# Kernel optimization log

Measured on AMD Instinct MI355X. Metric: run time of the kernel, lower is better.

Reference implementation:

```python
import jax, jax.numpy as jnp
import numpy as np
import math

N, E, LAT, MUL, HD = 20000, 160000, 128, 16, 32
H = LAT // HD          # 4 heads
D = 9                  # 0e+1o+2e spherical harmonics dim
SLICES = ((0, 1), (1, 4), (4, 9))
TPD = MUL * len(SLICES)


def _mlp(x, W1, b1, W2, b2):
    return jnp.dot(jax.nn.silu(jnp.dot(x, W1) + b1), W2) + b2


def _eq_linear(x, W):
    # block-diagonal per-l channel mixing: x [E, mul, D], W [n_l, mul, mul]
    return jnp.concatenate([jnp.einsum('ji,eim->ejm', W[l], x[:, :, s:t])
                            for l, (s, t) in enumerate(SLICES)], axis=-1)


def _residual(x, x_new, uc):
    co = jax.lax.rsqrt(uc * uc + 1.0)
    return co * x + (uc * co) * x_new


def _vec_rej(feat, dirs):
    d = dirs[:, None, :]
    return feat - (feat * d).sum(-1, keepdims=True) * d


def _so3_ln(x, eps=1e-8):
    # equivariant RMS layernorm per irrep block
    out = []
    for s, t in SLICES:
        blk = x[:, :, s:t]
        rms = jnp.sqrt((blk * blk).sum(-1).mean(-1) + eps)  # [N]
        out.append(blk / rms[:, None, None])
    return jnp.concatenate(out, axis=-1)


def _ln(x, g, b, eps=1e-5):
    mu = x.mean(-1, keepdims=True)
    var = ((x - mu) ** 2).mean(-1, keepdims=True)
    return (x - mu) * jax.lax.rsqrt(var + eps) * g + b


def _forward(h, X, t_ij, spharms, update_coeff, Wtq, Wtk, Wrs_W, Wrs_b, Wq_W, Wq_b, Wk_W, Wk_b, Wre_W, ln_g, ln_b, Wvu,
             gs_W1, gs_b1, gs_W2, gs_b2, gv_W1, gv_b1, gv_W2, gv_b2, gw_W1, gw_b1, gw_W2, gw_b2,
             gt_W1, gt_b1, gt_W2, gt_b2, gsp_W1, gsp_b1, gsp_W2, gsp_b2, md_W1, md_b1, md_W2, md_b2,
             mt_W1, mt_b1, mt_W2, mt_b2, gm_W1, gm_b1, gm_W2, gm_b2,
             edge_center, edge_neighbor, num_nodes):
    uc = update_coeff
    Xn = X[edge_neighbor]                                     # [E, mul, D]
    Xq = _vec_rej(_eq_linear(X[edge_center], Wtq), spharms)
    Xk = _vec_rej(_eq_linear(Xn, Wtk), -spharms)
    # CG scalar contraction (l x l -> 0e, uuu): normalized per-l dot product
    w = jnp.concatenate([(Xq[:, :, s:t] * Xk[:, :, s:t]).sum(-1) / math.sqrt(t - s)
                         for s, t in SLICES], axis=-1)        # [E, 3*mul]
    dt = _mlp(w, gw_W1, gw_b1, gw_W2, gw_b2) * _mlp(t_ij, gt_W1, gt_b1, gt_W2, gt_b2)
    t_ij = _residual(t_ij, dt, uc)
    h_i = h[edge_center]
    h_j = h[edge_neighbor]
    spatial = (t_ij @ Wrs_W + Wrs_b) * _mlp(h_j, gs_W1, gs_b1, gs_W2, gs_b2)
    En = t_ij.shape[0]
    q = (h_i @ Wq_W + Wq_b).reshape(En, H, HD)
    k = (h_j @ Wk_W + Wk_b).reshape(En, H, HD)
    v = _mlp(h_j, gv_W1, gv_b1, gv_W2, gv_b2)
    ta = jax.nn.silu(t_ij @ Wre_W).reshape(En, H, HD)
    alpha = (q * k * ta).sum(-1) / math.sqrt(HD)              # [E, H]
    amax = jax.ops.segment_max(alpha, edge_center, num_segments=num_nodes)
    ex = jnp.exp(alpha - amax[edge_center])
    den = jax.ops.segment_sum(ex, edge_center, num_segments=num_nodes)
    attn = ex / den[edge_center]                              # scatter_softmax
    sea = (attn[:, :, None] * v.reshape(En, H, HD)).reshape(En, LAT)
    combined = sea + spatial
    gates = _mlp(combined, gsp_W1, gsp_b1, gsp_W2, gsp_b2)
    o_s, o_d, o_t = gates[:, :LAT], gates[:, LAT:2 * LAT], gates[:, 2 * LAT:]
    dh = _ln(jax.ops.segment_sum(o_s, edge_center, num_segments=num_nodes), ln_g, ln_b)
    h = _residual(h, dh, uc)
    gd = _mlp(o_d, md_W1, md_b1, md_W2, md_b2)
    gtt = _mlp(o_t, mt_W1, mt_b1, mt_W2, mt_b2)
    dXij = gd[:, :, None] * spharms[:, None, :] + gtt[:, :, None] * Xn
    dX = _so3_ln(jax.ops.segment_sum(dXij, edge_center, num_segments=num_nodes))
    X = _residual(X, dX, uc)
    # EQFF
    Xp = jnp.einsum('nmi,mj->nji', X, Wvu)
    nrm = jnp.sqrt((Xp * Xp).sum(-1) + 1e-12)
    g = _mlp(jnp.concatenate([h, nrm], axis=-1), gm_W1, gm_b1, gm_W2, gm_b2)
    h = h + g[:, :LAT]
    X = X + g[:, LAT:, None] * Xp
    return h, X, t_ij


def setup_inputs() -> dict:
    key = jax.random.key(0)
    ks = jax.random.split(key, 24)

    def mk_mlp(k, din, dout):
        k1, k2 = jax.random.split(k)
        return (jax.random.normal(k1, (din, LAT)) / math.sqrt(din), jnp.zeros((LAT,)),
                jax.random.normal(k2, (LAT, dout)) / math.sqrt(LAT), jnp.zeros((dout,)))

    inp = {
        'h': jax.random.normal(ks[0], (N, LAT)),
        'X': jax.random.normal(ks[1], (N, MUL, D)),
        't_ij': jax.random.normal(ks[2], (E, LAT)),
        'spharms': jax.random.normal(ks[3], (E, D)),
        'update_coeff': jnp.ones((1,), dtype=jnp.float32),
        'Wtq': jax.random.normal(ks[4], (len(SLICES), MUL, MUL)) / math.sqrt(MUL),
        'Wtk': jax.random.normal(ks[5], (len(SLICES), MUL, MUL)) / math.sqrt(MUL),
        'Wrs_W': jax.random.normal(ks[6], (LAT, LAT)) / math.sqrt(LAT),
        'Wrs_b': jnp.zeros((LAT,)),
        'Wq_W': jax.random.normal(ks[7], (LAT, LAT)) / math.sqrt(LAT),
        'Wq_b': jnp.zeros((LAT,)),
        'Wk_W': jax.random.normal(ks[8], (LAT, LAT)) / math.sqrt(LAT),
        'Wk_b': jnp.zeros((LAT,)),
        'Wre_W': jax.random.normal(ks[9], (LAT, LAT)) / math.sqrt(LAT),
        'ln_g': jnp.ones((LAT,)),
        'ln_b': jnp.zeros((LAT,)),
        'Wvu': jax.random.normal(ks[10], (MUL, MUL)) / math.sqrt(MUL),
    }
    for name, din, dout, k in [('gs', LAT, LAT, ks[11]), ('gv', LAT, LAT, ks[12]), ('gw', TPD, LAT, ks[13]),
                               ('gt', LAT, LAT, ks[14]), ('gsp', LAT, 3 * LAT, ks[15]), ('md', LAT, MUL, ks[16]),
                               ('mt', LAT, MUL, ks[17]), ('gm', LAT + MUL, LAT + MUL, ks[18])]:
        W1, b1, W2, b2 = mk_mlp(k, din, dout)
        inp[name + '_W1'], inp[name + '_b1'], inp[name + '_W2'], inp[name + '_b2'] = W1, b1, W2, b2
    inp['edge_center'] = jax.random.randint(ks[19], (E,), 0, N)
    inp['edge_neighbor'] = jax.random.randint(ks[20], (E,), 0, N)
    inp['num_nodes'] = N
    return inp


def reference(h, X, t_ij, spharms, update_coeff, Wtq, Wtk, Wrs_W, Wrs_b, Wq_W, Wq_b, Wk_W, Wk_b, Wre_W, ln_g, ln_b, Wvu,
              gs_W1, gs_b1, gs_W2, gs_b2, gv_W1, gv_b1, gv_W2, gv_b2, gw_W1, gw_b1, gw_W2, gw_b2,
              gt_W1, gt_b1, gt_W2, gt_b2, gsp_W1, gsp_b1, gsp_W2, gsp_b2, md_W1, md_b1, md_W2, md_b2,
              mt_W1, mt_b1, mt_W2, mt_b2, gm_W1, gm_b1, gm_W2, gm_b2,
              edge_center, edge_neighbor, num_nodes):
    return _forward(h, X, t_ij, spharms, update_coeff, Wtq, Wtk, Wrs_W, Wrs_b, Wq_W, Wq_b, Wk_W, Wk_b, Wre_W, ln_g, ln_b, Wvu,
                    gs_W1, gs_b1, gs_W2, gs_b2, gv_W1, gv_b1, gv_W2, gv_b2, gw_W1, gw_b1, gw_W2, gw_b2,
                    gt_W1, gt_b1, gt_W2, gt_b2, gsp_W1, gsp_b1, gsp_W2, gsp_b2, md_W1, md_b1, md_W2, md_b2,
                    mt_W1, mt_b1, mt_W2, mt_b2, gm_W1, gm_b1, gm_W2, gm_b2,
                    edge_center, edge_neighbor, num_nodes)
```

## Files before the change

kernel.cpp:

```cpp
#include <hip/hip_runtime.h>
#include <math.h>

#define N_NODES 20000
#define E_EDGES 160000
#define LAT 128
#define MUL 16
#define DD 9
#define TPD 48

#define WS_Q      ((size_t)0)
#define WS_K      (WS_Q + (size_t)N_NODES*LAT)
#define WS_V      (WS_K + (size_t)N_NODES*LAT)
#define WS_S      (WS_V + (size_t)N_NODES*LAT)
#define WS_W48    (WS_S + (size_t)N_NODES*LAT)
#define WS_SPATB  (WS_W48 + (size_t)E_EDGES*TPD)
#define WS_ALPHA  (WS_SPATB + (size_t)E_EDGES*LAT/2)
#define WS_ZERO   (WS_ALPHA + (size_t)E_EDGES*4)
#define WS_AMAX   WS_ZERO
#define WS_DEN    (WS_AMAX + (size_t)N_NODES*4)
#define WS_HSUM   (WS_DEN + (size_t)N_NODES*4)
#define WS_NDX    (WS_HSUM + (size_t)N_NODES*LAT)
#define WS_END    (WS_NDX + (size_t)N_NODES*MUL*DD)
#define ZERO_CNT  (WS_END - WS_ZERO)
#define WS_WB     WS_END

#define WOFF_WQ   0
#define WOFF_WK   16384
#define WOFF_GV1  32768
#define WOFF_GV2  49152
#define WOFF_GS1  65536
#define WOFF_GS2  81920
#define WOFF_GW1  98304
#define WOFF_GW2  106496
#define WOFF_GT1  122880
#define WOFF_GT2  139264
#define WOFF_WRS  155648
#define WOFF_WRE  172032
#define WOFF_GSP1 188416
#define WOFF_GSP2 204800
#define WOFF_MD1  253952
#define WOFF_MD2  270336
#define WOFF_MT1  272384
#define WOFF_MT2  288768
#define WB_TOTAL  290816

#define DEVI __device__ __forceinline__

typedef short short8 __attribute__((ext_vector_type(8)));
typedef float f32x4 __attribute__((ext_vector_type(4)));

DEVI float silu_f(float x){ return x / (1.f + expf(-x)); }
DEVI unsigned int fmap(float x){ unsigned int b=__float_as_uint(x); return (b&0x80000000u)? ~b : (b|0x80000000u); }
DEVI float funmap(unsigned int u){ return (u&0x80000000u)? __uint_as_float(u&0x7fffffffu) : __uint_as_float(~u); }
DEVI unsigned short f2b(float f){ unsigned int u=__float_as_uint(f); return (unsigned short)((u + 0x7fffu + ((u>>16)&1u))>>16); }
DEVI float b2f(unsigned short u){ return __uint_as_float(((unsigned int)u)<<16); }

DEVI f32x4 mfma16(short8 a, short8 b, f32x4 c){
  return __builtin_amdgcn_mfma_f32_16x16x32_bf16(a,b,c,0,0,0);
}

template<int KB>
DEVI void mm_tile2(const unsigned short* act, int strideUS, const unsigned short* Wp,
                   int ntile, int m, int quad, f32x4* acc){
  const unsigned short* wp = Wp + (size_t)ntile*KB*512 + (size_t)quad*128 + m*8;
  const unsigned short* a0 = act + m*strideUS + quad*8;
  const unsigned short* a1 = a0 + 16*strideUS;
  #pragma unroll
  for (int kb=0;kb<KB;++kb){
    short8 bfr = *(const short8*)(wp + (size_t)kb*512);
    short8 af0 = *(const short8*)(a0 + kb*32);
    short8 af1 = *(const short8*)(a1 + kb*32);
    acc[0]=mfma16(af0,bfr,acc[0]);
    acc[1]=mfma16(af1,bfr,acc[1]);
  }
}

template<int KB>
DEVI void mm_tile1(const unsigned short* act, int strideUS, const unsigned short* Wp,
                   int mtbase, int m, int quad, f32x4& acc){
  const unsigned short* wp = Wp + (size_t)quad*128 + m*8;
  const unsigned short* a0 = act + (mtbase*16+m)*strideUS + quad*8;
  #pragma unroll
  for (int kb=0;kb<KB;++kb){
    short8 bfr = *(const short8*)(wp + (size_t)kb*512);
    short8 af  = *(const short8*)(a0 + kb*32);
    acc=mfma16(af,bfr,acc);
  }
}

template<int R, int KD, int LDSTRIDE>
DEVI void mm_acc(const float* src, const float* __restrict__ W, int wstride, int t, float* acc){
  #pragma unroll 2
  for (int k=0;k<KD;k+=4){
    float4 xv[R];
    #pragma unroll
    for (int r=0;r<R;++r) xv[r] = *(const float4*)(src + r*LDSTRIDE + k);
    #pragma unroll
    for (int kk=0;kk<4;++kk){
      float wk = W[(size_t)(k+kk)*wstride + t];
      #pragma unroll
      for (int r=0;r<R;++r) acc[r] += ((const float*)&xv[r])[kk]*wk;
    }
  }
}

__global__ void k0_zero(float* __restrict__ z){
  size_t i = (size_t)blockIdx.x*256 + threadIdx.x;
  if (i < ZERO_CNT) z[i] = 0.f;
}

__global__ __launch_bounds__(256) void k_pack(
  const float* __restrict__ Wq,const float* __restrict__ Wk,
  const float* __restrict__ gv1,const float* __restrict__ gv2,
  const float* __restrict__ gs1,const float* __restrict__ gs2,
  const float* __restrict__ gw1,const float* __restrict__ gw2,
  const float* __restrict__ gt1,const float* __restrict__ gt2,
  const float* __restrict__ Wrs,const float* __restrict__ Wre,
  const float* __restrict__ gsp1,const float* __restrict__ gsp2,
  const float* __restrict__ md1,const float* __restrict__ md2,
  const float* __restrict__ mt1,const float* __restrict__ mt2,
  unsigned short* __restrict__ dst)
{
  int i = blockIdx.x*256 + threadIdx.x;
  if (i >= WB_TOTAL) return;
  const int off[19] = {0,16384,32768,49152,65536,81920,98304,106496,122880,139264,
                       155648,172032,188416,204800,253952,270336,272384,288768,290816};
  int mi=0;
  while (i >= off[mi+1]) ++mi;
  int li = i - off[mi];
  int N = (mi==13)?384:((mi==15||mi==17)?16:128);
  int Ksrc = (mi==6)?48:128;
  int KB = (mi==6)?2:4;
  int j = li&7; int t = li>>3;
  int n_in = t&15; t>>=4;
  int quad = t&3; t>>=2;
  int k_block = t % KB; int n_tile = t / KB;
  int k = k_block*32 + quad*8 + j;
  int n = n_tile*16 + n_in;
  const float* src;
  switch(mi){
    case 0: src=Wq; break;  case 1: src=Wk; break;
    case 2: src=gv1; break; case 3: src=gv2; break;
    case 4: src=gs1; break; case 5: src=gs2; break;
    case 6: src=gw1; break; case 7: src=gw2; break;
    case 8: src=gt1; break; case 9: src=gt2; break;
    case 10: src=Wrs; break; case 11: src=Wre; break;
    case 12: src=gsp1; break; case 13: src=gsp2; break;
    case 14: src=md1; break; case 15: src=md2; break;
    default: src=(mi==16)?mt1:mt2; break;
  }
  float v = (k < Ksrc) ? src[(size_t)k*N + n] : 0.f;
  dst[i] = f2b(v);
}

__global__ __launch_bounds__(256) void k1_node(const float* __restrict__ h,
  const unsigned short* __restrict__ WB,
  const float* __restrict__ Wq_b,const float* __restrict__ Wk_b,
  const float* __restrict__ gv_b1,const float* __restrict__ gv_b2,
  const float* __restrict__ gs_b1,const float* __restrict__ gs_b2,
  float* __restrict__ ws)
{
  __shared__ __align__(16) unsigned short B0[32*136], B1[32*136];
  const int tid=threadIdx.x, lane=tid&63, w=tid>>6, m=lane&15, quad=lane>>4;
  const int n0=blockIdx.x*32;
  for (int idx=tid; idx<4096; idx+=256){ int r=idx>>7,c=idx&127;
    B0[r*136+c]=f2b(h[(size_t)(n0+r)*128+c]); }
  __syncthreads();
  f32x4 z4 = {0.f,0.f,0.f,0.f};
  { f32x4 acc[2][2]={{z4,z4},{z4,z4}};
    #pragma unroll
    for(int i=0;i<2;++i) mm_tile2<4>(B0,136,WB+WOFF_WQ, w*2+i, m, quad, acc[i]);
    #pragma unroll
    for(int i=0;i<2;++i){ int col=(w*2+i)*16+m; float bv=Wq_b[col];
      #pragma unroll
      for(int mt=0;mt<2;++mt)
        #pragma unroll
        for(int r=0;r<4;++r){ int row=mt*16+quad*4+r;
          ws[WS_Q+(size_t)(n0+row)*128+col]=acc[i][mt][r]+bv; } } }
  { f32x4 acc[2][2]={{z4,z4},{z4,z4}};
    #pragma unroll
    for(int i=0;i<2;++i) mm_tile2<4>(B0,136,WB+WOFF_WK, w*2+i, m, quad, acc[i]);
    #pragma unroll
    for(int i=0;i<2;++i){ int col=(w*2+i)*16+m; float bv=Wk_b[col];
      #pragma unroll
      for(int mt=0;mt<2;++mt)
        #pragma unroll
        for(int r=0;r<4;++r){ int row=mt*16+quad*4+r;
          ws[WS_K+(size_t)(n0+row)*128+col]=acc[i][mt][r]+bv; } } }
  { f32x4 acc[2][2]={{z4,z4},{z4,z4}};
    #pragma unroll
    for(int i=0;i<2;++i) mm_tile2<4>(B0,136,WB+WOFF_GV1, w*2+i, m, quad, acc[i]);
    #pragma unroll
    for(int i=0;i<2;++i){ int col=(w*2+i)*16+m; float bv=gv_b1[col];
      #pragma unroll
      for(int mt=0;mt<2;++mt)
        #pragma unroll
        for(int r=0;r<4;++r) B1[(mt*16+quad*4+r)*136+col]=f2b(silu_f(acc[i][mt][r]+bv)); } }
  __syncthreads();
  { f32x4 acc[2][2]={{z4,z4},{z4,z4}};
    #pragma unroll
    for(int i=0;i<2;++i) mm_tile2<4>(B1,136,WB+WOFF_GV2, w*2+i, m, quad, acc[i]);
    #pragma unroll
    for(int i=0;i<2;++i){ int col=(w*2+i)*16+m; float bv=gv_b2[col];
      #pragma unroll
      for(int mt=0;mt<2;++mt)
        #pragma unroll
        for(int r=0;r<4;++r){ int row=mt*16+quad*4+r;
          ws[WS_V+(size_t)(n0+row)*128+col]=acc[i][mt][r]+bv; } } }
  __syncthreads();
  { f32x4 acc[2][2]={{z4,z4},{z4,z4}};
    #pragma unroll
    for(int i=0;i<2;++i) mm_tile2<4>(B0,136,WB+WOFF_GS1, w*2+i, m, quad, acc[i]);
    #pragma unroll
    for(int i=0;i<2;++i){ int col=(w*2+i)*16+m; float bv=gs_b1[col];
      #pragma unroll
      for(int mt=0;mt<2;++mt)
        #pragma unroll
        for(int r=0;r<4;++r) B1[(mt*16+quad*4+r)*136+col]=f2b(silu_f(acc[i][mt][r]+bv)); } }
  __syncthreads();
  { f32x4 acc[2][2]={{z4,z4},{z4,z4}};
    #pragma unroll
    for(int i=0;i<2;++i) mm_tile2<4>(B1,136,WB+WOFF_GS2, w*2+i, m, quad, acc[i]);
    #pragma unroll
    for(int i=0;i<2;++i){ int col=(w*2+i)*16+m; float bv=gs_b2[col];
      #pragma unroll
      for(int mt=0;mt<2;++mt)
        #pragma unroll
        for(int r=0;r<4;++r){ int row=mt*16+quad*4+r;
          ws[WS_S+(size_t)(n0+row)*128+col]=acc[i][mt][r]+bv; } } }
}

__global__ __launch_bounds__(256) void k2_edge_w(
  const float* __restrict__ Xin, const float* __restrict__ sph,
  const float* __restrict__ Wtq, const float* __restrict__ Wtk,
  const int* __restrict__ ec, const int* __restrict__ en, float* __restrict__ ws)
{
  __shared__ float xc[16][144], xn[16][144], sphL[16][9];
  __shared__ float wq[768], wkk[768];
  __shared__ int ceI[16], nbI[16];
  const int tid=threadIdx.x, e0=blockIdx.x*16;
  if (tid<16){ ceI[tid]=ec[e0+tid]; nbI[tid]=en[e0+tid]; }
  for (int idx=tid; idx<768; idx+=256){ wq[idx]=Wtq[idx]; wkk[idx]=Wtk[idx]; }
  __syncthreads();
  for (int idx=tid; idx<2304; idx+=256){ int r=idx/144,c=idx%144;
    xc[r][c]=Xin[(size_t)ceI[r]*144+c]; xn[r][c]=Xin[(size_t)nbI[r]*144+c]; }
  if (tid<144){ int r=tid/9,c=tid%9; sphL[r][c]=sph[(size_t)(e0+r)*9+c]; }
  __syncthreads();
  const int el=tid>>4, j=tid&15;
  float xq[9], xk[9];
  const int ss[3]={0,1,4}, se[3]={1,4,9};
  #pragma unroll
  for (int l=0;l<3;++l){
    for (int mm2=ss[l]; mm2<se[l]; ++mm2){
      float aq=0.f, ak=0.f;
      #pragma unroll
      for (int i=0;i<16;++i){
        float wql = wq[l*256 + j*16 + i], wkl = wkk[l*256 + j*16 + i];
        aq += wql*xc[el][i*9+mm2];
        ak += wkl*xn[el][i*9+mm2];
      }
      xq[mm2]=aq; xk[mm2]=ak;
    }
  }
  float dq=0.f, dk=0.f;
  #pragma unroll
  for (int d=0; d<9; ++d){ dq += xq[d]*sphL[el][d]; dk += xk[d]*sphL[el][d]; }
  #pragma unroll
  for (int d=0; d<9; ++d){ xq[d] -= dq*sphL[el][d]; xk[d] -= dk*sphL[el][d]; }
  const float isc[3] = {1.f, 0.5773502691896258f, 0.4472135954999579f};
  #pragma unroll
  for (int l=0;l<3;++l){
    float s=0.f;
    for (int mm2=ss[l]; mm2<se[l]; ++mm2) s += xq[mm2]*xk[mm2];
    ws[WS_W48 + (size_t)(e0+el)*TPD + l*16 + j] = s*isc[l];
  }
}

__global__ __launch_bounds__(256) void k3_edge_t(
  const float* __restrict__ t_in, const int* __restrict__ ec, const int* __restrict__ en,
  const unsigned short* __restrict__ WB,
  const float* __restrict__ gw_b1,const float* __restrict__ gw_b2,
  const float* __restrict__ gt_b1,const float* __restrict__ gt_b2,
  const float* __restrict__ Wrs_b,
  const float* __restrict__ ucp, float* __restrict__ ws, float* __restrict__ outT)
{
  __shared__ __align__(16) unsigned short tin_b[32*136], hid_b[32*136], tnw_b[32*136], wb_b[32*72];
  __shared__ float qk[32*132];
  __shared__ int ceI[32], nbI[32];
  const int tid=threadIdx.x, lane=tid&63, w=tid>>6, m=lane&15, quad=lane>>4;
  const int e0=blockIdx.x*32;
  if (tid<32){ ceI[tid]=ec[e0+tid]; nbI[tid]=en[e0+tid]; }
  __syncthreads();
  const float* Qp=ws+WS_Q; const float* Kp=ws+WS_K;
  for (int idx=tid; idx<4096; idx+=256){
    int r=idx>>7, c=idx&127;
    tin_b[r*136+c] = f2b(t_in[(size_t)(e0+r)*128+c]);
    qk[r*132+c] = Qp[(size_t)ceI[r]*128+c]*Kp[(size_t)nbI[r]*128+c];
  }
  for (int idx=tid; idx<2048; idx+=256){
    int r=idx>>6, c=idx&63;
    wb_b[r*72+c] = (c<48)? f2b(ws[WS_W48+(size_t)(e0+r)*TPD+c]) : (unsigned short)0;
  }
  __syncthreads();
  const float uc=ucp[0], co=rsqrtf(uc*uc+1.f), ucco=uc*co;
  f32x4 z4 = {0.f,0.f,0.f,0.f};
  { f32x4 acc[2][2]={{z4,z4},{z4,z4}};
    #pragma unroll
    for(int i=0;i<2;++i) mm_tile2<2>(wb_b,72,WB+WOFF_GW1, w*2+i, m, quad, acc[i]);
    #pragma unroll
    for(int i=0;i<2;++i){ int col=(w*2+i)*16+m; float bv=gw_b1[col];
      #pragma unroll
      for(int mt=0;mt<2;++mt)
        #pragma unroll
        for(int r=0;r<4;++r) hid_b[(mt*16+quad*4+r)*136+col]=f2b(silu_f(acc[i][mt][r]+bv)); } }
  __syncthreads();
  f32x4 accw[2][2]={{z4,z4},{z4,z4}};
  #pragma unroll
  for(int i=0;i<2;++i) mm_tile2<4>(hid_b,136,WB+WOFF_GW2, w*2+i, m, quad, accw[i]);
  __syncthreads();
  { f32x4 acc[2][2]={{z4,z4},{z4,z4}};
    #pragma unroll
    for(int i=0;i<2;++i) mm_tile2<4>(tin_b,136,WB+WOFF_GT1, w*2+i, m, quad, acc[i]);
    #pragma unroll
    for(int i=0;i<2;++i){ int col=(w*2+i)*16+m; float bv=gt_b1[col];
      #pragma unroll
      for(int mt=0;mt<2;++mt)
        #pragma unroll
        for(int r=0;r<4;++r) hid_b[(mt*16+quad*4+r)*136+col]=f2b(silu_f(acc[i][mt][r]+bv)); } }
  __syncthreads();
  { f32x4 acct[2][2]={{z4,z4},{z4,z4}};
    #pragma unroll
    for(int i=0;i<2;++i) mm_tile2<4>(hid_b,136,WB+WOFF_GT2, w*2+i, m, quad, acct[i]);
    #pragma unroll
    for(int i=0;i<2;++i){ int col=(w*2+i)*16+m; float bw=gw_b2[col], bt=gt_b2[col];
      #pragma unroll
      for(int mt=0;mt<2;++mt)
        #pragma unroll
        for(int r=0;r<4;++r){ int row=mt*16+quad*4+r;
          float dt=(accw[i][mt][r]+bw)*(acct[i][mt][r]+bt);
          float tn=co*b2f(tin_b[row*136+col]) + ucco*dt;
          tnw_b[row*136+col]=f2b(tn);
          outT[(size_t)(e0+row)*128+col]=tn; } } }
  __syncthreads();
  unsigned short* spatB = (unsigned short*)(ws+WS_SPATB);
  { f32x4 acc[2][2]={{z4,z4},{z4,z4}};
    #pragma unroll
    for(int i=0;i<2;++i) mm_tile2<4>(tnw_b,136,WB+WOFF_WRS, w*2+i, m, quad, acc[i]);
    #pragma unroll
    for(int i=0;i<2;++i){ int col=(w*2+i)*16+m; float bv=Wrs_b[col];
      #pragma unroll
      for(int mt=0;mt<2;++mt)
        #pragma unroll
        for(int r=0;r<4;++r){ int row=mt*16+quad*4+r;
          float sv=ws[WS_S+(size_t)nbI[row]*128+col];
          spatB[(size_t)(e0+row)*128+col]=f2b((acc[i][mt][r]+bv)*sv); } } }
  { f32x4 acc[2][2]={{z4,z4},{z4,z4}};
    #pragma unroll
    for(int i=0;i<2;++i) mm_tile2<4>(tnw_b,136,WB+WOFF_WRE, w*2+i, m, quad, acc[i]);
    unsigned int* amaxu=(unsigned int*)(ws+WS_AMAX);
    #pragma unroll
    for(int mt=0;mt<2;++mt)
      #pragma unroll
      for(int r=0;r<4;++r){ int row=mt*16+quad*4+r;
        float p=0.f;
        #pragma unroll
        for(int i=0;i<2;++i){ int col=(w*2+i)*16+m;
          p += qk[row*132+col]*silu_f(acc[i][mt][r]); }
        p += __shfl_xor(p,1); p += __shfl_xor(p,2); p += __shfl_xor(p,4); p += __shfl_xor(p,8);
        if (m==0){
          float aval = p * 0.17677669529663687f;
          int e=e0+row;
          ws[WS_ALPHA+(size_t)e*4+w]=aval;
          atomicMax(&amaxu[(size_t)ceI[row]*4+w], fmap(aval));
        } } }
}

__global__ __launch_bounds__(256) void k4_softmax(const int* __restrict__ ec, float* __restrict__ ws){
  int i = blockIdx.x*256 + threadIdx.x;
  if (i >= E_EDGES*4) return;
  int e = i>>2, hh = i&3;
  int c = ec[e];
  float a = ws[WS_ALPHA + i];
  const unsigned int* amaxu = (const unsigned int*)(ws + WS_AMAX);
  float am = funmap(amaxu[(size_t)c*4+hh]);
  float exv = expf(a - am);
  ws[WS_ALPHA + i] = exv;
  atomicAdd(&ws[WS_DEN + (size_t)c*4 + hh], exv);
}

__global__ __launch_bounds__(256) void k5_edge_gate(
  const float* __restrict__ Xin, const float* __restrict__ sph,
  const int* __restrict__ ec, const int* __restrict__ en,
  const unsigned short* __restrict__ WB,
  const float* __restrict__ gsp_b1,const float* __restrict__ gsp_b2,
  const float* __restrict__ md_b1,const float* __restrict__ md_b2,
  const float* __restrict__ mt_b1,const float* __restrict__ mt_b2,
  float* __restrict__ ws)
{
  __shared__ __align__(16) unsigned short B0[32*136], B1[32*136], B2[32*136], B3[32*136];
  __shared__ float gdL[32*16], gtL[32*16], attnL[32*4];
  __shared__ int ceI[32], nbI[32];
  const int tid=threadIdx.x, lane=tid&63, w=tid>>6, m=lane&15, quad=lane>>4;
  const int e0=blockIdx.x*32;
  if (tid<32){ ceI[tid]=ec[e0+tid]; nbI[tid]=en[e0+tid]; }
  __syncthreads();
  if (tid<128){ int r=tid>>2, hh=tid&3;
    attnL[tid] = ws[WS_ALPHA+(size_t)(e0+r)*4+hh] / ws[WS_DEN+(size_t)ceI[r]*4+hh]; }
  __syncthreads();
  const float* Vp=ws+WS_V;
  const unsigned short* spatB=(const unsigned short*)(ws+WS_SPATB);
  for (int idx=tid; idx<4096; idx+=256){ int r=idx>>7,c=idx&127;
    float v = attnL[r*4+(c>>5)]*Vp[(size_t)nbI[r]*128+c] + b2f(spatB[(size_t)(e0+r)*128+c]);
    B0[r*136+c]=f2b(v); }
  __syncthreads();
  f32x4 z4 = {0.f,0.f,0.f,0.f};
  { f32x4 acc[2][2]={{z4,z4},{z4,z4}};
    #pragma unroll
    for(int i=0;i<2;++i) mm_tile2<4>(B0,136,WB+WOFF_GSP1, w*2+i, m, quad, acc[i]);
    #pragma unroll
    for(int i=0;i<2;++i){ int col=(w*2+i)*16+m; float bv=gsp_b1[col];
      #pragma unroll
      for(int mt=0;mt<2;++mt)
        #pragma unroll
        for(int r=0;r<4;++r) B1[(mt*16+quad*4+r)*136+col]=f2b(silu_f(acc[i][mt][r]+bv)); } }
  __syncthreads();
  { f32x4 acc[3][2][2];
    #pragma unroll
    for(int g2=0;g2<3;++g2)
      #pragma unroll
      for(int i=0;i<2;++i){ acc[g2][i][0]=z4; acc[g2][i][1]=z4; }
    #pragma unroll
    for(int g2=0;g2<3;++g2)
      #pragma unroll
      for(int i=0;i<2;++i)
        mm_tile2<4>(B1,136,WB+WOFF_GSP2, g2*8+w*2+i, m, quad, acc[g2][i]);
    float* hsum=ws+WS_HSUM;
    #pragma unroll
    for(int i=0;i<2;++i){ int col=(w*2+i)*16+m;
      float bS=gsp_b2[col], bD=gsp_b2[128+col], bT=gsp_b2[256+col];
      #pragma unroll
      for(int mt=0;mt<2;++mt)
        #pragma unroll
        for(int r=0;r<4;++r){ int row=mt*16+quad*4+r;
          atomicAdd(&hsum[(size_t)ceI[row]*128+col], acc[0][i][mt][r]+bS);
          B2[row*136+col]=f2b(acc[1][i][mt][r]+bD);
          B3[row*136+col]=f2b(acc[2][i][mt][r]+bT); } } }
  __syncthreads();
  { f32x4 acc[2][2]={{z4,z4},{z4,z4}};
    #pragma unroll
    for(int i=0;i<2;++i) mm_tile2<4>(B2,136,WB+WOFF_MD1, w*2+i, m, quad, acc[i]);
    #pragma unroll
    for(int i=0;i<2;++i){ int col=(w*2+i)*16+m; float bv=md_b1[col];
      #pragma unroll
      for(int mt=0;mt<2;++mt)
        #pragma unroll
        for(int r=0;r<4;++r) B0[(mt*16+quad*4+r)*136+col]=f2b(silu_f(acc[i][mt][r]+bv)); } }
  __syncthreads();
  { f32x4 acc[2][2]={{z4,z4},{z4,z4}};
    #pragma unroll
    for(int i=0;i<2;++i) mm_tile2<4>(B3,136,WB+WOFF_MT1, w*2+i, m, quad, acc[i]);
    #pragma unroll
    for(int i=0;i<2;++i){ int col=(w*2+i)*16+m; float bv=mt_b1[col];
      #pragma unroll
      for(int mt=0;mt<2;++mt)
        #pragma unroll
        for(int r=0;r<4;++r) B2[(mt*16+quad*4+r)*136+col]=f2b(silu_f(acc[i][mt][r]+bv)); } }
  __syncthreads();
  { if (w<2){
      f32x4 a=z4; mm_tile1<4>(B0,136,WB+WOFF_MD2, w, m, quad, a);
      #pragma unroll
      for(int r=0;r<4;++r) gdL[(w*16+quad*4+r)*16+m]=a[r]+md_b2[m];
    } else {
      f32x4 a=z4; mm_tile1<4>(B2,136,WB+WOFF_MT2, w-2, m, quad, a);
      #pragma unroll
      for(int r=0;r<4;++r) gtL[((w-2)*16+quad*4+r)*16+m]=a[r]+mt_b2[m];
    } }
  __syncthreads();
  float* ndx=ws+WS_NDX;
  for (int idx=tid; idx<4608; idx+=256){
    int r=idx/144, c=idx-r*144; int mm2=c/9, d=c-mm2*9;
    float val = gdL[r*16+mm2]*sph[(size_t)(e0+r)*9+d] + gtL[r*16+mm2]*Xin[(size_t)nbI[r]*144+c];
    atomicAdd(&ndx[(size_t)ceI[r]*144+c], val);
  }
}

__global__ __launch_bounds__(128) void k6_node(
  const float* __restrict__ h, const float* __restrict__ Xin,
  const float* __restrict__ ln_g,const float* __restrict__ ln_b,
  const float* __restrict__ Wvu,
  const float* __restrict__ gm_W1,const float* __restrict__ gm_b1,
  const float* __restrict__ gm_W2,const float* __restrict__ gm_b2,
  const float* __restrict__ ucp, const float* __restrict__ ws,
  float* __restrict__ outH, float* __restrict__ outX)
{
  __shared__ float cat[4][144], dxb[4][144], xnw[4][144], xp[4][144], hid[4][LAT];
  __shared__ float red[4][2][2], rinv[4][3], gX[4][16], wvu[256];
  const int t=threadIdx.x, n0=blockIdx.x*4;
  const float* hsum=ws+WS_HSUM; const float* ndx=ws+WS_NDX;
  const float uc=ucp[0], co=rsqrtf(uc*uc+1.f), ucco=uc*co;
  for (int idx=t; idx<256; idx+=128) wvu[idx]=Wvu[idx];
  for (int idx=t; idx<576; idx+=128){ int r=idx/144,c=idx%144; dxb[r][c]=ndx[(size_t)(n0+r)*144+c]; }
  float xv_[4];
  #pragma unroll
  for (int r=0;r<4;++r){
    float x=hsum[(size_t)(n0+r)*LAT+t]; xv_[r]=x;
    float s=x, ss=x*x;
    for (int off=32; off; off>>=1){ s+=__shfl_down(s,off,64); ss+=__shfl_down(ss,off,64); }
    if ((t&63)==0){ red[r][t>>6][0]=s; red[r][t>>6][1]=ss; }
  }
  __syncthreads();
  #pragma unroll
  for (int r=0;r<4;++r){
    float s=red[r][0][0]+red[r][1][0], ss=red[r][0][1]+red[r][1][1];
    float mu=s*(1.f/128.f), var=ss*(1.f/128.f)-mu*mu;
    float dh=(xv_[r]-mu)*rsqrtf(var+1e-5f)*ln_g[t]+ln_b[t];
    cat[r][t]=co*h[(size_t)(n0+r)*LAT+t]+ucco*dh;
  }
  if (t<12){
    int r=t/3, l=t-r*3;
    int s0 = (l==0)?0:((l==1)?1:4);
    int s1 = (l==0)?1:((l==1)?4:9);
    float sum=0.f;
    for (int mm2=0;mm2<16;++mm2)
      for (int d=s0;d<s1;++d){ float v=dxb[r][mm2*9+d]; sum+=v*v; }
    rinv[r][l]=rsqrtf(sum*(1.f/16.f)+1e-8f);
  }
  __syncthreads();
  for (int idx=t; idx<144; idx+=128){
    int d=idx%9; int l=(d==0)?0:((d<4)?1:2);
    #pragma unroll
    for (int r=0;r<4;++r)
      xnw[r][idx]=co*Xin[(size_t)(n0+r)*144+idx]+ucco*dxb[r][idx]*rinv[r][l];
  }
  __syncthreads();
  for (int idx=t; idx<144; idx+=128){
    int j=idx/9, i=idx-j*9;
    #pragma unroll
    for (int r=0;r<4;++r){
      float a=0.f;
      #pragma unroll
      for (int mm2=0;mm2<16;++mm2) a+=xnw[r][mm2*9+i]*wvu[mm2*16+j];
      xp[r][idx]=a;
    }
  }
  __syncthreads();
  if (t<64){ int r=t>>4, j=t&15; float s=1e-12f;
    #pragma unroll
    for (int i=0;i<9;++i){ float v=xp[r][j*9+i]; s+=v*v; }
    cat[r][128+j]=sqrtf(s); }
  __syncthreads();
  { float acc[4]; float b=gm_b1[t];
    #pragma unroll
    for(int r=0;r<4;++r)acc[r]=b;
    mm_acc<4,144,144>(&cat[0][0],gm_W1,LAT,t,acc);
    #pragma unroll
    for(int r=0;r<4;++r) hid[r][t]=silu_f(acc[r]); }
  __syncthreads();
  { float acc[4]; float b=gm_b2[t];
    #pragma unroll
    for(int r=0;r<4;++r)acc[r]=b;
    mm_acc<4,LAT,LAT>(&hid[0][0],gm_W2,144,t,acc);
    #pragma unroll
    for(int r=0;r<4;++r) outH[(size_t)(n0+r)*LAT+t]=cat[r][t]+acc[r]; }
  if (t<16){ float acc[4]; float b=gm_b2[128+t];
    #pragma unroll
    for(int r=0;r<4;++r)acc[r]=b;
    for (int k=0;k<LAT;++k){ float wk=gm_W2[(size_t)k*144+128+t];
      #pragma unroll
      for(int r=0;r<4;++r) acc[r]+=hid[r][k]*wk; }
    #pragma unroll
    for(int r=0;r<4;++r) gX[r][t]=acc[r]; }
  __syncthreads();
  for (int idx=t; idx<144; idx+=128){
    int j=idx/9;
    #pragma unroll
    for (int r=0;r<4;++r)
      outX[(size_t)(n0+r)*144+idx]=xnw[r][idx]+gX[r][j]*xp[r][idx];
  }
}

extern "C" void kernel_launch(void* const* d_in, const int* in_sizes, int n_in,
                              void* d_out, int out_size, void* d_ws, size_t ws_size,
                              hipStream_t stream)
{
  const float* h      = (const float*)d_in[0];
  const float* X      = (const float*)d_in[1];
  const float* t_ij   = (const float*)d_in[2];
  const float* sph    = (const float*)d_in[3];
  const float* ucp    = (const float*)d_in[4];
  const float* Wtq    = (const float*)d_in[5];
  const float* Wtk    = (const float*)d_in[6];
  const float* Wrs_W  = (const float*)d_in[7];
  const float* Wrs_b  = (const float*)d_in[8];
  const float* Wq_W   = (const float*)d_in[9];
  const float* Wq_b   = (const float*)d_in[10];
  const float* Wk_W   = (const float*)d_in[11];
  const float* Wk_b   = (const float*)d_in[12];
  const float* Wre_W  = (const float*)d_in[13];
  const float* ln_g   = (const float*)d_in[14];
  const float* ln_b   = (const float*)d_in[15];
  const float* Wvu    = (const float*)d_in[16];
  const float* gs_W1=(const float*)d_in[17], *gs_b1=(const float*)d_in[18],
             *gs_W2=(const float*)d_in[19], *gs_b2=(const float*)d_in[20];
  const float* gv_W1=(const float*)d_in[21], *gv_b1=(const float*)d_in[22],
             *gv_W2=(const float*)d_in[23], *gv_b2=(const float*)d_in[24];
  const float* gw_W1=(const float*)d_in[25], *gw_b1=(const float*)d_in[26],
             *gw_W2=(const float*)d_in[27], *gw_b2=(const float*)d_in[28];
  const float* gt_W1=(const float*)d_in[29], *gt_b1=(const float*)d_in[30],
             *gt_W2=(const float*)d_in[31], *gt_b2=(const float*)d_in[32];
  const float* gsp_W1=(const float*)d_in[33], *gsp_b1=(const float*)d_in[34],
             *gsp_W2=(const float*)d_in[35], *gsp_b2=(const float*)d_in[36];
  const float* md_W1=(const float*)d_in[37], *md_b1=(const float*)d_in[38],
             *md_W2=(const float*)d_in[39], *md_b2=(const float*)d_in[40];
  const float* mt_W1=(const float*)d_in[41], *mt_b1=(const float*)d_in[42],
             *mt_W2=(const float*)d_in[43], *mt_b2=(const float*)d_in[44];
  const float* gm_W1=(const float*)d_in[45], *gm_b1=(const float*)d_in[46],
             *gm_W2=(const float*)d_in[47], *gm_b2=(const float*)d_in[48];
  const int* ec = (const int*)d_in[49];
  const int* en = (const int*)d_in[50];
  (void)in_sizes; (void)n_in; (void)out_size; (void)ws_size;

  float* ws   = (float*)d_ws;
  unsigned short* WB = (unsigned short*)(ws + WS_WB);
  float* outH = (float*)d_out;
  float* outX = outH + (size_t)N_NODES*LAT;
  float* outT = outX + (size_t)N_NODES*MUL*DD;

  k0_zero<<<dim3((unsigned)((ZERO_CNT+255)/256)), dim3(256), 0, stream>>>(ws + WS_ZERO);
  k_pack<<<dim3((WB_TOTAL+255)/256), dim3(256), 0, stream>>>(
      Wq_W,Wk_W, gv_W1,gv_W2, gs_W1,gs_W2, gw_W1,gw_W2, gt_W1,gt_W2,
      Wrs_W,Wre_W, gsp_W1,gsp_W2, md_W1,md_W2, mt_W1,mt_W2, WB);
  k1_node<<<dim3(N_NODES/32), dim3(256), 0, stream>>>(h, WB, Wq_b, Wk_b,
      gv_b1,gv_b2, gs_b1,gs_b2, ws);
  k2_edge_w<<<dim3(E_EDGES/16), dim3(256), 0, stream>>>(X, sph, Wtq, Wtk, ec, en, ws);
  k3_edge_t<<<dim3(E_EDGES/32), dim3(256), 0, stream>>>(t_ij, ec, en, WB,
      gw_b1,gw_b2, gt_b1,gt_b2, Wrs_b, ucp, ws, outT);
  k4_softmax<<<dim3((E_EDGES*4)/256), dim3(256), 0, stream>>>(ec, ws);
  k5_edge_gate<<<dim3(E_EDGES/32), dim3(256), 0, stream>>>(X, sph, ec, en, WB,
      gsp_b1,gsp_b2, md_b1,md_b2, mt_b1,mt_b2, ws);
  k6_node<<<dim3(N_NODES/4), dim3(128), 0, stream>>>(h, X, ln_g, ln_b, Wvu,
      gm_W1,gm_b1,gm_W2,gm_b2, ucp, ws, outH, outX);
}
```

Before: 813.4 us.

## Accumulate node scatter sums with packed bf16 atomics and use fast exp

The hsum and ndx scatter reductions change from fp32 atomicAdd to packed bf16x2 global atomics. Each atomic now carries two adjacent columns, which halves the atomic count and the bytes of contended traffic. The node kernel reads the accumulators back as bf16. silu and softmax also switch to __expf. Summing many edges into bf16 accumulators loses a lot of precision and may break the tolerance check.

```diff
diff --git a/kernel.cpp b/kernel.cpp
--- a/kernel.cpp
+++ b/kernel.cpp
@@ -49,11 +49,15 @@
 typedef short short8 __attribute__((ext_vector_type(8)));
 typedef float f32x4 __attribute__((ext_vector_type(4)));
 
-DEVI float silu_f(float x){ return x / (1.f + expf(-x)); }
+DEVI float silu_f(float x){ return x / (1.f + __expf(-x)); }
 DEVI unsigned int fmap(float x){ unsigned int b=__float_as_uint(x); return (b&0x80000000u)? ~b : (b|0x80000000u); }
 DEVI float funmap(unsigned int u){ return (u&0x80000000u)? __uint_as_float(u&0x7fffffffu) : __uint_as_float(~u); }
 DEVI unsigned short f2b(float f){ unsigned int u=__float_as_uint(f); return (unsigned short)((u + 0x7fffu + ((u>>16)&1u))>>16); }
 DEVI float b2f(unsigned short u){ return __uint_as_float(((unsigned int)u)<<16); }
+
+DEVI void atom_pk(unsigned short* p, unsigned int pk){
+  asm volatile("global_atomic_pk_add_bf16 %0, %1, off" :: "v"(p), "v"(pk) : "memory");
+}
 
 DEVI f32x4 mfma16(short8 a, short8 b, f32x4 c){
   return __builtin_amdgcn_mfma_f32_16x16x32_bf16(a,b,c,0,0,0);
@@ -383,7 +387,7 @@
   float a = ws[WS_ALPHA + i];
   const unsigned int* amaxu = (const unsigned int*)(ws + WS_AMAX);
   float am = funmap(amaxu[(size_t)c*4+hh]);
-  float exv = expf(a - am);
+  float exv = __expf(a - am);
   ws[WS_ALPHA + i] = exv;
   atomicAdd(&ws[WS_DEN + (size_t)c*4 + hh], exv);
 }
@@ -434,7 +438,7 @@
       #pragma unroll
       for(int i=0;i<2;++i)
         mm_tile2<4>(B1,136,WB+WOFF_GSP2, g2*8+w*2+i, m, quad, acc[g2][i]);
-    float* hsum=ws+WS_HSUM;
+    unsigned short* hsumB=(unsigned short*)(ws+WS_HSUM);
     #pragma unroll
     for(int i=0;i<2;++i){ int col=(w*2+i)*16+m;
       float bS=gsp_b2[col], bD=gsp_b2[128+col], bT=gsp_b2[256+col];
@@ -442,7 +446,12 @@
       for(int mt=0;mt<2;++mt)
         #pragma unroll
         for(int r=0;r<4;++r){ int row=mt*16+quad*4+r;
-          atomicAdd(&hsum[(size_t)ceI[row]*128+col], acc[0][i][mt][r]+bS);
+          float vS = acc[0][i][mt][r]+bS;
+          float vO = __shfl_xor(vS,1);
+          if(!(m&1)){
+            unsigned int pk = ((unsigned int)f2b(vO)<<16) | (unsigned int)f2b(vS);
+            atom_pk(hsumB + (size_t)ceI[row]*128 + col, pk);
+          }
           B2[row*136+col]=f2b(acc[1][i][mt][r]+bD);
           B3[row*136+col]=f2b(acc[2][i][mt][r]+bT); } } }
   __syncthreads();
@@ -476,11 +485,17 @@
       for(int r=0;r<4;++r) gtL[((w-2)*16+quad*4+r)*16+m]=a[r]+mt_b2[m];
     } }
   __syncthreads();
-  float* ndx=ws+WS_NDX;
-  for (int idx=tid; idx<4608; idx+=256){
-    int r=idx/144, c=idx-r*144; int mm2=c/9, d=c-mm2*9;
-    float val = gdL[r*16+mm2]*sph[(size_t)(e0+r)*9+d] + gtL[r*16+mm2]*Xin[(size_t)nbI[r]*144+c];
-    atomicAdd(&ndx[(size_t)ceI[r]*144+c], val);
+  unsigned short* ndxB=(unsigned short*)(ws+WS_NDX);
+  for (int idx=tid; idx<2304; idx+=256){
+    int r=idx/72, p=idx-r*72; int c0=2*p, c1=c0+1;
+    int mm0=c0/9, d0=c0-mm0*9;
+    int mm1=c1/9, d1=c1-mm1*9;
+    const float* sphE = sph + (size_t)(e0+r)*9;
+    const float* xrow = Xin + (size_t)nbI[r]*144;
+    float v0 = gdL[r*16+mm0]*sphE[d0] + gtL[r*16+mm0]*xrow[c0];
+    float v1 = gdL[r*16+mm1]*sphE[d1] + gtL[r*16+mm1]*xrow[c1];
+    unsigned int pk = ((unsigned int)f2b(v1)<<16) | (unsigned int)f2b(v0);
+    atom_pk(ndxB + (size_t)ceI[r]*144 + c0, pk);
   }
 }
 
@@ -496,14 +511,15 @@
   __shared__ float cat[4][144], dxb[4][144], xnw[4][144], xp[4][144], hid[4][LAT];
   __shared__ float red[4][2][2], rinv[4][3], gX[4][16], wvu[256];
   const int t=threadIdx.x, n0=blockIdx.x*4;
-  const float* hsum=ws+WS_HSUM; const float* ndx=ws+WS_NDX;
+  const unsigned short* hsumB=(const unsigned short*)(ws+WS_HSUM);
+  const unsigned short* ndxB =(const unsigned short*)(ws+WS_NDX);
   const float uc=ucp[0], co=rsqrtf(uc*uc+1.f), ucco=uc*co;
   for (int idx=t; idx<256; idx+=128) wvu[idx]=Wvu[idx];
-  for (int idx=t; idx<576; idx+=128){ int r=idx/144,c=idx%144; dxb[r][c]=ndx[(size_t)(n0+r)*144+c]; }
+  for (int idx=t; idx<576; idx+=128){ int r=idx/144,c=idx%144; dxb[r][c]=b2f(ndxB[(size_t)(n0+r)*144+c]); }
   float xv_[4];
   #pragma unroll
   for (int r=0;r<4;++r){
-    float x=hsum[(size_t)(n0+r)*LAT+t]; xv_[r]=x;
+    float x=b2f(hsumB[(size_t)(n0+r)*LAT+t]); xv_[r]=x;
     float s=x, ss=x*x;
     for (int off=32; off; off>>=1){ s+=__shfl_down(s,off,64); ss+=__shfl_down(ss,off,64); }
     if ((t&63)==0){ red[r][t>>6][0]=s; red[r][t>>6][1]=ss; }
```

New measurement: 777.6 us. 1.05x faster.
